# Kernel tuning notes

Measured on AMD Instinct MI355X. Metric: run time of the kernel, lower is better.

The kernel has to match this reference:

```python
import jax, jax.numpy as jnp
import numpy as np

B, C, N = 2, 32, 4096
EPS = 1e-5


def _batchnorm1d(x, gamma, bias):
    # BatchNorm1d in training mode: stats over (batch, spatial) per channel, biased var
    mean = x.mean(axis=(0, 2), keepdims=True)
    var = x.var(axis=(0, 2), keepdims=True)
    return (x - mean) * jax.lax.rsqrt(var + EPS) * gamma[None, :, None] + bias[None, :, None]


def setup_inputs() -> dict:
    key = jax.random.key(0)
    k1, k2, k3 = jax.random.split(key, 3)
    Feature = jax.random.normal(k1, (B, C, N), dtype=jnp.float32)
    gamma = jnp.ones((C,), dtype=jnp.float32)
    bn_bias = jnp.zeros((C,), dtype=jnp.float32)
    alpha = jax.random.uniform(k2, (), dtype=jnp.float32)
    beta = jax.random.uniform(k3, (), dtype=jnp.float32)
    return {"Feature": Feature, "gamma": gamma, "bn_bias": bn_bias, "alpha": alpha, "beta": beta}


def reference(Feature, gamma, bn_bias, alpha, beta):
    a = Feature                                   # [B, C, N]
    # --- PAM: BN + ReLU prologue, then spatial N x N attention ---
    f = jax.nn.relu(_batchnorm1d(Feature, gamma, bn_bias))
    cb = jnp.einsum('bcn,bcm->bnm', f, f)         # c^T c : [B, N, N]
    s = jax.nn.softmax(cb, axis=1)                # softmax over dim=1 (as in source)
    e_p = jnp.einsum('bcn,bmn->bcm', f, s)        # c @ s^T : [B, C, N]
    pam = alpha * e_p + a
    # --- CAM: channel C x C attention, softmax over batch axis (dim=0 as in source) ---
    aa = jnp.einsum('bcn,bdn->bdc', a, a)         # matmul(a, a^T).permute(0,2,1) : [B, C, C]
    x = jax.nn.softmax(aa, axis=0)
    e_c = jnp.einsum('bji,bjn->bin', x, a)        # x^T @ a : [B, C, N]
    cam = beta * e_c + a
    return pam + cam
```

## Files before the change

### kernel.cpp

```cpp
#include <hip/hip_runtime.h>
#include <math.h>


#define BB 2
#define CC 32
#define NN 4096
#define EPSV 1e-5f

typedef short short8 __attribute__((ext_vector_type(8)));
typedef float f32x4 __attribute__((ext_vector_type(4)));

#define OFF_FNC  0
#define OFF_FCN  131072
#define OFF_M    262144
#define OFF_XW   270336
#define OFF_AAP  272384
#define OFF_S1P  305152
#define OFF_S2P  305408
#define OFF_Z    305664

__device__ inline ushort f2bf(float x) {
    uint u = __float_as_uint(x);
    uint r = u + 0x7FFFu + ((u >> 16) & 1u);
    return (ushort)(r >> 16);
}
__device__ inline float bf2f(ushort h) { return __uint_as_float(((uint)h) << 16); }
__device__ inline uint packbf(float lo, float hi) {
    return (__float_as_uint(hi) & 0xFFFF0000u) | (__float_as_uint(lo) >> 16);
}

__global__ void __launch_bounds__(256) k_pre(const float* __restrict__ x,
                                             float* __restrict__ ws) {
    __shared__ float smem[4352];
    const int blk = blockIdx.x, t = threadIdx.x;
    const int lane = t & 63, wv = t >> 6;
    if (blk < 256) {
        const int c = blk & 31, chunk = blk >> 5;
        const int i0 = chunk * 1024;
        const int b = i0 >> 12, n0 = i0 & (NN - 1);
        const float4 v = *(const float4*)(x + ((size_t)(b * CC + c)) * NN + n0 + t * 4);
        float s  = v.x + v.y + v.z + v.w;
        float s2 = v.x * v.x + v.y * v.y + v.z * v.z + v.w * v.w;
        for (int off = 32; off; off >>= 1) { s += __shfl_down(s, off); s2 += __shfl_down(s2, off); }
        if (lane == 0) { smem[wv] = s; smem[4 + wv] = s2; }
        __syncthreads();
        if (t == 0) {
            ws[OFF_S1P + chunk * 32 + c] = smem[0] + smem[1] + smem[2] + smem[3];
            ws[OFF_S2P + chunk * 32 + c] = smem[4] + smem[5] + smem[6] + smem[7];
        }
    } else {
        const int blk2 = blk - 256;
        const int b = blk2 >> 4, chnk = blk2 & 15;
        const int nb = chnk * 256;
        const int d = t >> 3, cg4 = (t & 7) * 4;
        float a0 = 0.f, a1 = 0.f, a2 = 0.f, a3 = 0.f;
        for (int it = 0; it < 2; ++it) {
            __syncthreads();
            for (int li = t; li < 4096; li += 256) {
                const int row = li >> 7, col = li & 127;
                smem[row * 132 + col] = x[((size_t)(b * CC + row)) * NN + nb + it * 128 + col];
            }
            __syncthreads();
            for (int k = 0; k < 128; ++k) {
                const float vd = smem[d * 132 + k];
                a0 += smem[(cg4 + 0) * 132 + k] * vd;
                a1 += smem[(cg4 + 1) * 132 + k] * vd;
                a2 += smem[(cg4 + 2) * 132 + k] * vd;
                a3 += smem[(cg4 + 3) * 132 + k] * vd;
            }
        }
        float* dst = ws + OFF_AAP + ((size_t)((b * 16 + chnk) * CC + d)) * CC + cg4;
        dst[0] = a0; dst[1] = a1; dst[2] = a2; dst[3] = a3;
    }
}

__global__ void __launch_bounds__(256) k_makef(const float* __restrict__ x,
                                               const float* __restrict__ gamma,
                                               const float* __restrict__ bias,
                                               float* __restrict__ ws) {
    __shared__ float ssc[CC], ssh[CC];
    const int blk = blockIdx.x, t = threadIdx.x;
    if (t < CC) {
        float S1 = 0.f, S2 = 0.f;
        #pragma unroll
        for (int k = 0; k < 8; ++k) { S1 += ws[OFF_S1P + k * 32 + t]; S2 += ws[OFF_S2P + k * 32 + t]; }
        const float mean = S1 * (1.f / (BB * NN));
        const float var = S2 * (1.f / (BB * NN)) - mean * mean;
        const float sc = gamma[t] * rsqrtf(var + EPSV);
        ssc[t] = sc; ssh[t] = bias[t] - mean * sc;
    }
    ws[OFF_Z + blk * 256 + t] = 0.f;
    __syncthreads();
    const int idx = blk * 256 + t;
    const int b = idx >> 12, n = idx & (NN - 1);
    union { ushort us[CC]; short8 v[4]; } row;
    float msum = 0.f;
    #pragma unroll
    for (int c = 0; c < CC; ++c) {
        const float v = x[((size_t)(b * CC + c)) * NN + n];
        const float f = fmaxf(v * ssc[c] + ssh[c], 0.f);
        const ushort h = f2bf(f);
        const float fr = bf2f(h);
        msum += fr * fr;
        row.us[c] = h;
        ((ushort*)(ws + OFF_FCN))[((size_t)(b * CC + c)) * NN + n] = h;
    }
    short8* dst = (short8*)((ushort*)(ws + OFF_FNC) + (size_t)idx * CC);
    dst[0] = row.v[0]; dst[1] = row.v[1]; dst[2] = row.v[2]; dst[3] = row.v[3];
    ws[OFF_M + idx] = msum;
}

__global__ void __launch_bounds__(256) k_zpass(float* __restrict__ ws) {
    const int blk = blockIdx.x, t = threadIdx.x;
    if (blk == 2048) {
        for (int li = t; li < CC * CC; li += 256) {
            const int i = li >> 5, j = li & 31;
            float q0 = 0.f, q1 = 0.f;
            for (int cchunk = 0; cchunk < 16; ++cchunk) {
                q0 += ws[OFF_AAP + ((size_t)((0 * 16 + cchunk) * CC + j)) * CC + i];
                q1 += ws[OFF_AAP + ((size_t)((1 * 16 + cchunk) * CC + j)) * CC + i];
            }
            const float mx = fmaxf(q0, q1);
            const float e0 = __expf(q0 - mx), e1 = __expf(q1 - mx);
            const float inv = 1.f / (e0 + e1);
            ws[OFF_XW + 0 * 1024 + i * 32 + j] = e0 * inv;
            ws[OFF_XW + 1 * 1024 + i * 32 + j] = e1 * inv;
        }
        return;
    }
    const ushort* fnc = (const ushort*)(ws + OFF_FNC);
    const int lane = t & 63, wv = t >> 6;
    const int ml = lane & 15, kg = lane >> 4;
    const f32x4 fzero = {0.f, 0.f, 0.f, 0.f};
    const int b = blk >> 10;
    const int rem = blk & 1023;
    const int ng = rem >> 5;
    const int mch = rem & 31;
    const int nbA = ng * 128 + wv * 16, nbB = nbA + 64;
    const short8 bfA = *(const short8*)(fnc + ((size_t)(b * NN + nbA + ml)) * CC + kg * 8);
    const short8 bfB = *(const short8*)(fnc + ((size_t)(b * NN + nbB + ml)) * CC + kg * 8);
    const float MA = ws[OFF_M + b * NN + nbA + ml];
    const float MB = ws[OFF_M + b * NN + nbB + ml];
    float zA = 0.f, zB = 0.f;
    const int m0 = mch * 128;
    for (int mm = m0; mm < m0 + 128; mm += 16) {
        const short8 af = *(const short8*)(fnc + ((size_t)(b * NN + mm + ml)) * CC + kg * 8);
        f32x4 dA = __builtin_amdgcn_mfma_f32_16x16x32_bf16(af, bfA, fzero, 0, 0, 0);
        f32x4 dB = __builtin_amdgcn_mfma_f32_16x16x32_bf16(af, bfB, fzero, 0, 0, 0);
        zA += __expf(dA[0] - MA) + __expf(dA[1] - MA) + __expf(dA[2] - MA) + __expf(dA[3] - MA);
        zB += __expf(dB[0] - MB) + __expf(dB[1] - MB) + __expf(dB[2] - MB) + __expf(dB[3] - MB);
    }
    zA += __shfl_xor(zA, 16); zA += __shfl_xor(zA, 32);
    zB += __shfl_xor(zB, 16); zB += __shfl_xor(zB, 32);
    if (lane < 16) {
        atomicAdd(ws + OFF_Z + b * NN + nbA + ml, zA);
        atomicAdd(ws + OFF_Z + b * NN + nbB + ml, zB);
    }
}

__global__ void __launch_bounds__(512) k_epfinal(const float* __restrict__ x,
                                                 const float* __restrict__ alpha_p,
                                                 const float* __restrict__ beta_p,
                                                 const float* __restrict__ ws,
                                                 float* __restrict__ out) {
    __shared__ float red[8][512];
    __shared__ float sxw[CC * 33];
    __shared__ float sa[CC * 16];
    const ushort* fnc = (const ushort*)(ws + OFF_FNC);
    const ushort* fcn = (const ushort*)(ws + OFF_FCN);
    const int blk = blockIdx.x, t = threadIdx.x;
    const int lane = t & 63, wv = t >> 6;
    const int ml = lane & 15, kg = lane >> 4;
    const f32x4 fzero = {0.f, 0.f, 0.f, 0.f};
    const int b = blk >> 8, mg = blk & 255;
    const int mb = mg * 16;

    { const int j = t >> 4, mcol = t & 15;
      sa[j * 16 + mcol] = x[((size_t)(b * CC + j)) * NN + mb + mcol]; }
    for (int li = t; li < CC * CC; li += 512)
        sxw[(li >> 5) * 33 + (li & 31)] = ws[OFF_XW + b * 1024 + li];

    const short8 bm = *(const short8*)(fnc + ((size_t)(b * NN + mb + ml)) * CC + kg * 8);
    f32x4 acc0 = fzero, acc1 = fzero;
    const float* Mp = ws + OFF_M + b * NN;
    const float* Zp = ws + OFF_Z + b * NN;
    const int n0beg = wv * 512;
    for (int n0 = n0beg; n0 < n0beg + 512; n0 += 32) {
        const short8 an0 = *(const short8*)(fnc + ((size_t)(b * NN + n0      + ml)) * CC + kg * 8);
        const short8 an1 = *(const short8*)(fnc + ((size_t)(b * NN + n0 + 16 + ml)) * CC + kg * 8);
        f32x4 d0 = __builtin_amdgcn_mfma_f32_16x16x32_bf16(an0, bm, fzero, 0, 0, 0);
        f32x4 d1 = __builtin_amdgcn_mfma_f32_16x16x32_bf16(an1, bm, fzero, 0, 0, 0);
        const float4 M0 = *(const float4*)(Mp + n0 + kg * 4);
        const float4 M1 = *(const float4*)(Mp + n0 + 16 + kg * 4);
        const float4 Z0 = *(const float4*)(Zp + n0 + kg * 4);
        const float4 Z1 = *(const float4*)(Zp + n0 + 16 + kg * 4);
        const float w00 = __expf(d0[0] - M0.x) * __builtin_amdgcn_rcpf(Z0.x);
        const float w01 = __expf(d0[1] - M0.y) * __builtin_amdgcn_rcpf(Z0.y);
        const float w02 = __expf(d0[2] - M0.z) * __builtin_amdgcn_rcpf(Z0.z);
        const float w03 = __expf(d0[3] - M0.w) * __builtin_amdgcn_rcpf(Z0.w);
        const float w10 = __expf(d1[0] - M1.x) * __builtin_amdgcn_rcpf(Z1.x);
        const float w11 = __expf(d1[1] - M1.y) * __builtin_amdgcn_rcpf(Z1.y);
        const float w12 = __expf(d1[2] - M1.z) * __builtin_amdgcn_rcpf(Z1.z);
        const float w13 = __expf(d1[3] - M1.w) * __builtin_amdgcn_rcpf(Z1.w);
        const uint p0 = packbf(w00, w01), p1 = packbf(w02, w03);
        const uint q0 = packbf(w10, w11), q1 = packbf(w12, w13);
        union { uint u[4]; short8 s; } wf;
        {
            const int s0 = (((kg & 1) << 1) + 0) * 16 + ml;
            const int s1 = (((kg & 1) << 1) + 1) * 16 + ml;
            const uint vp0 = __shfl(p0, s0), vp1 = __shfl(p1, s0);
            const uint vp2 = __shfl(p0, s1), vp3 = __shfl(p1, s1);
            const uint vq0 = __shfl(q0, s0), vq1 = __shfl(q1, s0);
            const uint vq2 = __shfl(q0, s1), vq3 = __shfl(q1, s1);
            const bool hi = (kg >= 2);
            wf.u[0] = hi ? vq0 : vp0; wf.u[1] = hi ? vq1 : vp1;
            wf.u[2] = hi ? vq2 : vp2; wf.u[3] = hi ? vq3 : vp3;
        }
        const short8 a20 = *(const short8*)(fcn + ((size_t)(b * CC + ml))      * NN + n0 + kg * 8);
        const short8 a21 = *(const short8*)(fcn + ((size_t)(b * CC + 16 + ml)) * NN + n0 + kg * 8);
        acc0 = __builtin_amdgcn_mfma_f32_16x16x32_bf16(a20, wf.s, acc0, 0, 0, 0);
        acc1 = __builtin_amdgcn_mfma_f32_16x16x32_bf16(a21, wf.s, acc1, 0, 0, 0);
    }
    #pragma unroll
    for (int r = 0; r < 4; ++r) {
        red[wv][(kg * 4 + r) * 16 + ml]      = acc0[r];
        red[wv][(16 + kg * 4 + r) * 16 + ml] = acc1[r];
    }
    __syncthreads();
    float ep = 0.f;
    #pragma unroll
    for (int w = 0; w < 8; ++w) ep += red[w][t];
    const float alpha = *alpha_p, beta = *beta_p;
    const int c = t >> 4, m2 = t & 15;
    float ec = 0.f;
    #pragma unroll
    for (int j = 0; j < CC; ++j) ec += sxw[c * 33 + j] * sa[j * 16 + m2];
    const float av = sa[c * 16 + m2];
    out[((size_t)(b * CC + c)) * NN + mb + m2] = alpha * ep + beta * ec + 2.f * av;
}

extern "C" void kernel_launch(void* const* d_in, const int* in_sizes, int n_in,
                              void* d_out, int out_size, void* d_ws, size_t ws_size,
                              hipStream_t stream) {
    const float* x     = (const float*)d_in[0];
    const float* gamma = (const float*)d_in[1];
    const float* bias  = (const float*)d_in[2];
    const float* alpha = (const float*)d_in[3];
    const float* beta  = (const float*)d_in[4];
    float* out = (float*)d_out;
    float* ws  = (float*)d_ws;

    hipLaunchKernelGGL(k_pre,     dim3(288),  dim3(256), 0, stream, x, ws);
    hipLaunchKernelGGL(k_makef,   dim3(32),   dim3(256), 0, stream, x, gamma, bias, ws);
    hipLaunchKernelGGL(k_zpass,   dim3(2049), dim3(256), 0, stream, ws);
    hipLaunchKernelGGL(k_epfinal, dim3(512),  dim3(512), 0, stream, x, alpha, beta, ws, out);
}
```

Measured before the change: 129.1 us.

## Prescale features by sqrt(log2 e) for exp2, widen makef grid, stage M/Z in LDS

```diff
diff --git a/kernel.cpp b/kernel.cpp
--- a/kernel.cpp
+++ b/kernel.cpp
@@ -6,6 +6,7 @@
 #define CC 32
 #define NN 4096
 #define EPSV 1e-5f
+#define SQL2E 1.2011224087864498f
 
 typedef short short8 __attribute__((ext_vector_type(8)));
 typedef float f32x4 __attribute__((ext_vector_type(4)));
@@ -79,7 +80,10 @@
                                                const float* __restrict__ bias,
                                                float* __restrict__ ws) {
     __shared__ float ssc[CC], ssh[CC];
-    const int blk = blockIdx.x, t = threadIdx.x;
+    __shared__ ushort tS[CC][18];
+    const int blk = blockIdx.x, t = threadIdx.x;
+    const int base = blk * 16;
+    const int b = base >> 12, n0 = base & (NN - 1);
     if (t < CC) {
         float S1 = 0.f, S2 = 0.f;
         #pragma unroll
@@ -89,25 +93,35 @@
         const float sc = gamma[t] * rsqrtf(var + EPSV);
         ssc[t] = sc; ssh[t] = bias[t] - mean * sc;
     }
-    ws[OFF_Z + blk * 256 + t] = 0.f;
-    __syncthreads();
-    const int idx = blk * 256 + t;
-    const int b = idx >> 12, n = idx & (NN - 1);
-    union { ushort us[CC]; short8 v[4]; } row;
-    float msum = 0.f;
-    #pragma unroll
-    for (int c = 0; c < CC; ++c) {
-        const float v = x[((size_t)(b * CC + c)) * NN + n];
-        const float f = fmaxf(v * ssc[c] + ssh[c], 0.f);
-        const ushort h = f2bf(f);
-        const float fr = bf2f(h);
-        msum += fr * fr;
-        row.us[c] = h;
-        ((ushort*)(ws + OFF_FCN))[((size_t)(b * CC + c)) * NN + n] = h;
-    }
-    short8* dst = (short8*)((ushort*)(ws + OFF_FNC) + (size_t)idx * CC);
-    dst[0] = row.v[0]; dst[1] = row.v[1]; dst[2] = row.v[2]; dst[3] = row.v[3];
-    ws[OFF_M + idx] = msum;
+    __syncthreads();
+    {
+        const int c = t >> 3, cp = t & 7;
+        const float2 v = *(const float2*)(x + ((size_t)(b * CC + c)) * NN + n0 + 2 * cp);
+        const float f0 = fmaxf(v.x * ssc[c] + ssh[c], 0.f);
+        const float f1 = fmaxf(v.y * ssc[c] + ssh[c], 0.f);
+        const ushort h0u = f2bf(f0), h1u = f2bf(f1);
+        ((uint*)((ushort*)(ws + OFF_FCN) + ((size_t)(b * CC + c)) * NN + n0))[cp] =
+            (uint)h0u | ((uint)h1u << 16);
+        const ushort h0s = f2bf(f0 * SQL2E), h1s = f2bf(f1 * SQL2E);
+        tS[c][2 * cp]     = h0s;
+        tS[c][2 * cp + 1] = h1s;
+    }
+    __syncthreads();
+    if (t < 64) {
+        const int col = t >> 2, q = t & 3;
+        union { ushort us[8]; short8 v; } r;
+        #pragma unroll
+        for (int j = 0; j < 8; ++j) r.us[j] = tS[q * 8 + j][col];
+        *(short8*)((ushort*)(ws + OFF_FNC) + ((size_t)(base + col)) * CC + q * 8) = r.v;
+    } else if (t < 80) {
+        const int col = t - 64;
+        float msum = 0.f;
+        #pragma unroll
+        for (int c = 0; c < CC; ++c) { const float fs = bf2f(tS[c][col]); msum += fs * fs; }
+        ws[OFF_M + base + col] = msum;
+    } else if (t < 96) {
+        ws[OFF_Z + blk * 16 + (t - 80)] = 0.f;
+    }
 }
 
 __global__ void __launch_bounds__(256) k_zpass(float* __restrict__ ws) {
@@ -147,8 +161,8 @@
         const short8 af = *(const short8*)(fnc + ((size_t)(b * NN + mm + ml)) * CC + kg * 8);
         f32x4 dA = __builtin_amdgcn_mfma_f32_16x16x32_bf16(af, bfA, fzero, 0, 0, 0);
         f32x4 dB = __builtin_amdgcn_mfma_f32_16x16x32_bf16(af, bfB, fzero, 0, 0, 0);
-        zA += __expf(dA[0] - MA) + __expf(dA[1] - MA) + __expf(dA[2] - MA) + __expf(dA[3] - MA);
-        zB += __expf(dB[0] - MB) + __expf(dB[1] - MB) + __expf(dB[2] - MB) + __expf(dB[3] - MB);
+        zA += exp2f(dA[0] - MA) + exp2f(dA[1] - MA) + exp2f(dA[2] - MA) + exp2f(dA[3] - MA);
+        zB += exp2f(dB[0] - MB) + exp2f(dB[1] - MB) + exp2f(dB[2] - MB) + exp2f(dB[3] - MB);
     }
     zA += __shfl_xor(zA, 16); zA += __shfl_xor(zA, 32);
     zB += __shfl_xor(zB, 16); zB += __shfl_xor(zB, 32);
@@ -164,6 +178,8 @@
                                                  const float* __restrict__ ws,
                                                  float* __restrict__ out) {
     __shared__ float red[8][512];
+    __shared__ float sM[NN];
+    __shared__ float sZi[NN];
     __shared__ float sxw[CC * 33];
     __shared__ float sa[CC * 16];
     const ushort* fnc = (const ushort*)(ws + OFF_FNC);
@@ -175,33 +191,44 @@
     const int b = blk >> 8, mg = blk & 255;
     const int mb = mg * 16;
 
-    { const int j = t >> 4, mcol = t & 15;
-      sa[j * 16 + mcol] = x[((size_t)(b * CC + j)) * NN + mb + mcol]; }
-    for (int li = t; li < CC * CC; li += 512)
-        sxw[(li >> 5) * 33 + (li & 31)] = ws[OFF_XW + b * 1024 + li];
+    {
+        const float* Mp = ws + OFF_M + b * NN;
+        const float* Zp = ws + OFF_Z + b * NN;
+        #pragma unroll
+        for (int i = t; i < NN / 4; i += 512) {
+            const float4 z = *(const float4*)(Zp + i * 4);
+            const float4 m = *(const float4*)(Mp + i * 4);
+            ((float4*)sZi)[i] = make_float4(__builtin_amdgcn_rcpf(z.x), __builtin_amdgcn_rcpf(z.y),
+                                            __builtin_amdgcn_rcpf(z.z), __builtin_amdgcn_rcpf(z.w));
+            ((float4*)sM)[i] = m;
+        }
+        const int j = t >> 4, mcol = t & 15;
+        sa[j * 16 + mcol] = x[((size_t)(b * CC + j)) * NN + mb + mcol];
+        for (int li = t; li < CC * CC; li += 512)
+            sxw[(li >> 5) * 33 + (li & 31)] = ws[OFF_XW + b * 1024 + li];
+    }
+    __syncthreads();
 
     const short8 bm = *(const short8*)(fnc + ((size_t)(b * NN + mb + ml)) * CC + kg * 8);
     f32x4 acc0 = fzero, acc1 = fzero;
-    const float* Mp = ws + OFF_M + b * NN;
-    const float* Zp = ws + OFF_Z + b * NN;
     const int n0beg = wv * 512;
     for (int n0 = n0beg; n0 < n0beg + 512; n0 += 32) {
         const short8 an0 = *(const short8*)(fnc + ((size_t)(b * NN + n0      + ml)) * CC + kg * 8);
         const short8 an1 = *(const short8*)(fnc + ((size_t)(b * NN + n0 + 16 + ml)) * CC + kg * 8);
         f32x4 d0 = __builtin_amdgcn_mfma_f32_16x16x32_bf16(an0, bm, fzero, 0, 0, 0);
         f32x4 d1 = __builtin_amdgcn_mfma_f32_16x16x32_bf16(an1, bm, fzero, 0, 0, 0);
-        const float4 M0 = *(const float4*)(Mp + n0 + kg * 4);
-        const float4 M1 = *(const float4*)(Mp + n0 + 16 + kg * 4);
-        const float4 Z0 = *(const float4*)(Zp + n0 + kg * 4);
-        const float4 Z1 = *(const float4*)(Zp + n0 + 16 + kg * 4);
-        const float w00 = __expf(d0[0] - M0.x) * __builtin_amdgcn_rcpf(Z0.x);
-        const float w01 = __expf(d0[1] - M0.y) * __builtin_amdgcn_rcpf(Z0.y);
-        const float w02 = __expf(d0[2] - M0.z) * __builtin_amdgcn_rcpf(Z0.z);
-        const float w03 = __expf(d0[3] - M0.w) * __builtin_amdgcn_rcpf(Z0.w);
-        const float w10 = __expf(d1[0] - M1.x) * __builtin_amdgcn_rcpf(Z1.x);
-        const float w11 = __expf(d1[1] - M1.y) * __builtin_amdgcn_rcpf(Z1.y);
-        const float w12 = __expf(d1[2] - M1.z) * __builtin_amdgcn_rcpf(Z1.z);
-        const float w13 = __expf(d1[3] - M1.w) * __builtin_amdgcn_rcpf(Z1.w);
+        const float4 M0 = *(const float4*)(sM + n0 + kg * 4);
+        const float4 M1 = *(const float4*)(sM + n0 + 16 + kg * 4);
+        const float4 Z0 = *(const float4*)(sZi + n0 + kg * 4);
+        const float4 Z1 = *(const float4*)(sZi + n0 + 16 + kg * 4);
+        const float w00 = exp2f(d0[0] - M0.x) * Z0.x;
+        const float w01 = exp2f(d0[1] - M0.y) * Z0.y;
+        const float w02 = exp2f(d0[2] - M0.z) * Z0.z;
+        const float w03 = exp2f(d0[3] - M0.w) * Z0.w;
+        const float w10 = exp2f(d1[0] - M1.x) * Z1.x;
+        const float w11 = exp2f(d1[1] - M1.y) * Z1.y;
+        const float w12 = exp2f(d1[2] - M1.z) * Z1.z;
+        const float w13 = exp2f(d1[3] - M1.w) * Z1.w;
         const uint p0 = packbf(w00, w01), p1 = packbf(w02, w03);
         const uint q0 = packbf(w10, w11), q1 = packbf(w12, w13);
         union { uint u[4]; short8 s; } wf;
@@ -251,7 +278,7 @@
     float* ws  = (float*)d_ws;
 
     hipLaunchKernelGGL(k_pre,     dim3(288),  dim3(256), 0, stream, x, ws);
-    hipLaunchKernelGGL(k_makef,   dim3(32),   dim3(256), 0, stream, x, gamma, bias, ws);
+    hipLaunchKernelGGL(k_makef,   dim3(512),  dim3(256), 0, stream, x, gamma, bias, ws);
     hipLaunchKernelGGL(k_zpass,   dim3(2049), dim3(256), 0, stream, ws);
     hipLaunchKernelGGL(k_epfinal, dim3(512),  dim3(512), 0, stream, x, alpha, beta, ws, out);
 }
```

New measurement: 124.8 us. 3.3% less time.
